# Optimization experiments

Hardware: AMD Instinct MI355X
Metric: run time of the kernel (lower is better)

The kernel has to match this reference:

```python
import jax, jax.numpy as jnp
import numpy as np

N = 100_000      # nodes
E = 1_600_000    # edges (avg degree 16)
D = 128          # emb_dim
L = 2            # num_layer
BN_EPS = 1e-5


def setup_inputs() -> dict:
    key = jax.random.key(0)
    ks = jax.random.split(key, 16)
    s = 0.05
    inp = {
        # int inputs
        "x": jax.random.randint(ks[0], (N, 9), 0, 2),
        "z": jax.random.randint(ks[1], (N,), 0, 1000),
        "edge_index": jax.random.randint(ks[2], (2, E), 0, N),
        "edge_attr": jax.random.randint(ks[3], (E, 3), 0, 2),
        # learned params
        "atom_emb": jax.random.normal(ks[4], (9, 119, D), jnp.float32) * s,  # padded stacked AtomEncoder tables
        "z_emb": jax.random.normal(ks[5], (1000, D), jnp.float32) * s,
        "bond_emb": jax.random.normal(ks[6], (L, 3, 6, D), jnp.float32) * s,  # padded BondEncoder tables per layer
        "eps": jnp.zeros((L,), jnp.float32),
        "W1": jax.random.normal(ks[7], (L, D, 2 * D), jnp.float32) * s,
        "b1": jnp.zeros((L, 2 * D), jnp.float32),
        "g1": jnp.ones((L, 2 * D), jnp.float32),
        "be1": jnp.zeros((L, 2 * D), jnp.float32),
        "W2": jax.random.normal(ks[8], (L, 2 * D, D), jnp.float32) * s,
        "b2": jnp.zeros((L, D), jnp.float32),
        "bng": jnp.ones((L, D), jnp.float32),
        "bnb": jnp.zeros((L, D), jnp.float32),
    }
    return inp


def _batchnorm(h, g, b):
    # training-mode BatchNorm1d: batch stats, biased variance
    m = h.mean(axis=0)
    v = h.var(axis=0)
    return (h - m) * jax.lax.rsqrt(v + BN_EPS) * g + b


def _multi_embed(tables, idx):
    # tables: [F, V, D], idx: [N, F] -> sum_f tables[f][idx[:, f]]  -> [N, D]
    return jax.vmap(lambda t, i: t[i], in_axes=(0, 1))(tables, idx).sum(axis=0)


def reference(x, z, edge_index, edge_attr, atom_emb, z_emb, bond_emb, eps,
              W1, b1, g1, be1, W2, b2, bng, bnb):
    src, dst = edge_index[0], edge_index[1]
    # h0 = AtomEncoder(x) + z_embedding(z)
    h = _multi_embed(atom_emb, x) + z_emb[z]
    for l in range(L):
        # GINConv: bond encode -> gather -> relu message -> scatter-add -> MLP
        e_emb = _multi_embed(bond_emb[l], edge_attr)          # [E, D]
        msg = jax.nn.relu(h[src] + e_emb)                      # [E, D]
        agg = jax.ops.segment_sum(msg, dst, num_segments=N)    # [N, D]
        pre = (1.0 + eps[l]) * h + agg
        hid = jax.nn.relu(_batchnorm(pre @ W1[l] + b1[l], g1[l], be1[l]))
        hconv = hid @ W2[l] + b2[l]
        h = _batchnorm(hconv, bng[l], bnb[l])
        if l < L - 1:
            h = jax.nn.relu(h)   # dropout ratio 0 -> identity
    return h
```

## Files before the change

### kernel.cpp

```cpp
#include <hip/hip_runtime.h>

#define D 128
#define BN_EPS 1e-5f
#define NSUB 1024
#define CAP2 2048
#define NCOPY 64

typedef __attribute__((ext_vector_type(8))) short short8;
typedef __attribute__((ext_vector_type(4))) float floatx4;

__device__ __forceinline__ float bf2f(unsigned short u) {
    unsigned int x = ((unsigned int)u) << 16;
    return __builtin_bit_cast(float, x);
}
__device__ __forceinline__ unsigned short f2bf(float f) {
    unsigned int x = __builtin_bit_cast(unsigned int, f);
    x = x + 0x7FFFu + ((x >> 16) & 1u);
    return (unsigned short)(x >> 16);
}
__device__ __forceinline__ int magdiv(unsigned int x, unsigned long long magic) {
    return (int)(((unsigned long long)x * magic) >> 44);
}

__global__ __launch_bounds__(256)
void partition_kernel(const int* __restrict__ ei, const int* __restrict__ ea,
                      unsigned int* __restrict__ subL, int* __restrict__ tail2,
                      int E, int N, unsigned long long magic, int ntiles, int nblocks) {
    __shared__ int lcnt[1024], lbase[1024];
    const int tid = threadIdx.x;
    for (int tile = blockIdx.x; tile < ntiles; tile += nblocks) {
        const int tb = tile * 4096;
#pragma unroll
        for (int i = 0; i < 4; ++i) lcnt[tid + i * 256] = 0;
        __syncthreads();
        int sub[16];
        unsigned int entry[16];
#pragma unroll
        for (int j = 0; j < 16; ++j) {
            int e = tb + j * 256 + tid;
            if (e < E) {
                int dst = ei[E + e];
                int c = (ea[3 * e] * 6 + ea[3 * e + 1]) * 6 + ea[3 * e + 2];
                int k = magdiv((unsigned)dst * 1024u, magic);
                int lo = (int)(((long long)k * N + 1023) >> 10);
                sub[j] = k;
                entry[j] = (unsigned int)ei[e] | ((unsigned int)c << 17) |
                           ((unsigned int)(dst - lo) << 25);
                atomicAdd(&lcnt[k], 1);
            } else {
                sub[j] = -1;
            }
        }
        __syncthreads();
#pragma unroll
        for (int i = 0; i < 4; ++i) {
            int k = tid + i * 256;
            int c = lcnt[k];
            if (c) lbase[k] = atomicAdd(&tail2[k], c);
            lcnt[k] = 0;
        }
        __syncthreads();
#pragma unroll
        for (int j = 0; j < 16; ++j) {
            if (sub[j] >= 0) {
                int k = sub[j];
                int pos = lbase[k] + atomicAdd(&lcnt[k], 1);
                if (pos < CAP2) subL[(size_t)k * CAP2 + pos] = entry[j];
            }
        }
        __syncthreads();
    }
}

__global__ __launch_bounds__(1024)
void subscan_kernel(const int* __restrict__ tail2, int* __restrict__ subbase,
                    int* __restrict__ offsets, int N) {
    const int tid = threadIdx.x, lane = tid & 63, wid = tid >> 6;
    int v = min(tail2[tid], CAP2);
    int s = v;
#pragma unroll
    for (int off = 1; off < 64; off <<= 1) {
        int t = __shfl_up(s, off, 64);
        if (lane >= off) s += t;
    }
    __shared__ int ws[16];
    if (lane == 63) ws[wid] = s;
    __syncthreads();
    if (wid == 0) {
        int w = (lane < 16) ? ws[lane] : 0;
#pragma unroll
        for (int off = 1; off < 16; off <<= 1) {
            int t = __shfl_up(w, off, 64);
            if (lane >= off) w += t;
        }
        if (lane < 16) ws[lane] = w;
    }
    __syncthreads();
    int excl = (wid ? ws[wid - 1] : 0) + s - v;
    subbase[tid] = excl;
    if (tid == 1023) offsets[N] = excl + v;
}

__global__ __launch_bounds__(256)
void sort_setup_kernel(const unsigned int* __restrict__ subL, const int* __restrict__ tail2,
                       const int* __restrict__ subbase, int* __restrict__ offsets,
                       int* __restrict__ bucket, int N,
                       const int* __restrict__ x, const int* __restrict__ z,
                       const float* __restrict__ atom_emb, const float* __restrict__ z_emb,
                       unsigned short* __restrict__ hb, int nbNode,
                       const float* __restrict__ bond_emb, float* __restrict__ comb,
                       const float* __restrict__ W1, unsigned short* __restrict__ w1p,
                       const float* __restrict__ W2, unsigned short* __restrict__ w2p) {
    __shared__ int cnt[128], loff[128], wsum[4];
    __shared__ unsigned int sorted[CAP2];
    const int tid = threadIdx.x;
    if (blockIdx.x < NSUB) {
        const int k = blockIdx.x;
        const int lane = tid & 63, wid = tid >> 6;
        const int len = min(tail2[k], CAP2);
        const int base = subbase[k];
        const int lo = (int)(((long long)k * N + 1023) >> 10);
        const int hi = (int)(((long long)(k + 1) * N + 1023) >> 10);
        const int nn = hi - lo;
        const unsigned int* src = subL + (size_t)k * CAP2;

        if (tid < 128) cnt[tid] = 0;
        __syncthreads();
        for (int i = tid; i < len; i += 256) atomicAdd(&cnt[src[i] >> 25], 1);
        __syncthreads();
        int v = (tid < 128) ? cnt[tid] : 0;
        int s = v;
#pragma unroll
        for (int off = 1; off < 64; off <<= 1) {
            int t = __shfl_up(s, off, 64);
            if (lane >= off) s += t;
        }
        if (lane == 63) wsum[wid] = s;
        __syncthreads();
        if (tid < 128) loff[tid] = ((wid == 1) ? wsum[0] : 0) + s - v;
        __syncthreads();
        if (tid < nn) offsets[lo + tid] = base + loff[tid];
        if (tid < 128) cnt[tid] = 0;
        __syncthreads();
        for (int i = tid; i < len; i += 256) {
            unsigned int e = src[i];
            int ld = e >> 25;
            int pos = loff[ld] + atomicAdd(&cnt[ld], 1);
            sorted[pos] = e & 0x1FFFFFFu;
        }
        __syncthreads();
        for (int i = tid; i < len; i += 256) bucket[base + i] = (int)sorted[i];
        return;
    }
    const int b = blockIdx.x - NSUB;
    if (b < nbNode) {
        int gid = b * 256 + tid;
        int node = gid >> 5;
        if (node >= N) return;
        int d0 = (gid & 31) * 4;
        float4 acc = *(const float4*)(z_emb + (size_t)z[node] * D + d0);
#pragma unroll
        for (int f = 0; f < 9; ++f) {
            int v = x[node * 9 + f];
            const float4 t = *(const float4*)(atom_emb + (size_t)(f * 119 + v) * D + d0);
            acc.x += t.x; acc.y += t.y; acc.z += t.z; acc.w += t.w;
        }
        ushort4 o;
        o.x = f2bf(acc.x); o.y = f2bf(acc.y); o.z = f2bf(acc.z); o.w = f2bf(acc.w);
        *(ushort4*)(hb + (size_t)node * D + d0) = o;
    } else if (b < nbNode + 216) {
        int t = (b - nbNode) * 256 + tid;
        int layer = t / (216 * D);
        int idx = t - layer * (216 * D);
        int c = idx >> 7, d = idx & 127;
        int a0 = c / 36, a1 = (c / 6) % 6, a2 = c % 6;
        const float* bb = bond_emb + (size_t)layer * 3 * 6 * D;
        float v = bb[(0 * 6 + a0) * D + d] + bb[(1 * 6 + a1) * D + d] + bb[(2 * 6 + a2) * D + d];
        comb[(size_t)layer * 216 * D + idx] = v;
    } else {
        int isW2 = (b >= nbNode + 216 + 256);
        int t = (b - nbNode - 216 - (isW2 ? 256 : 0)) * 256 + tid;
        int layer = t >> 15;
        int idx = t & 32767;
        int logN = isW2 ? 7 : 8;
        int NCOLS = 1 << logN;
        int k = idx >> logN, n = idx & (NCOLS - 1);
        int k0 = k >> 5, kq = k & 31, q = kq >> 3, j = kq & 7;
        int tt = n >> 4, ln = n & 15;
        size_t dest = (((size_t)k0 * (NCOLS >> 4) + tt) << 9) + ((q << 4) + ln) * 8 + j;
        const float* W = (isW2 ? W2 : W1) + (size_t)layer * 32768;
        unsigned short* Wp = (isW2 ? w2p : w1p) + (size_t)layer * 32768;
        Wp[dest] = f2bf(W[idx]);
    }
}

__global__ __launch_bounds__(256)
void gather_reduce_kernel(const int* __restrict__ offsets, const int* __restrict__ bucket,
                          const float* __restrict__ comb,
                          const unsigned short* __restrict__ hb,
                          const float* __restrict__ eps_l,
                          unsigned short* __restrict__ pre, int N) {
    int gid = blockIdx.x * blockDim.x + threadIdx.x;
    int node = gid >> 4;
    if (node >= N) return;
    int d0 = (gid & 15) * 8;

    union U8 { int4 i; unsigned short u[8]; };
    union C8 { float4 v[2]; float f[8]; };
    float s = 1.0f + eps_l[0];
    float a[8];
    {
        U8 hv; hv.i = *(const int4*)(hb + (size_t)node * D + d0);
#pragma unroll
        for (int j = 0; j < 8; ++j) a[j] = bf2f(hv.u[j]) * s;
    }
    const int beg = offsets[node], end = offsets[node + 1];
    for (int p = beg; p < end; p += 4) {
        int rem = end - p;
        int pk0 = bucket[p];
        int pk1 = bucket[rem > 1 ? p + 1 : p];
        int pk2 = bucket[rem > 2 ? p + 2 : p];
        int pk3 = bucket[rem > 3 ? p + 3 : p];
        U8 h0, h1, h2, h3;
        C8 c0, c1, c2, c3;
        h0.i = *(const int4*)(hb + (size_t)(pk0 & 0x1FFFF) * D + d0);
        c0.v[0] = *(const float4*)(comb + (size_t)(pk0 >> 17) * D + d0);
        c0.v[1] = *(const float4*)(comb + (size_t)(pk0 >> 17) * D + d0 + 4);
        h1.i = *(const int4*)(hb + (size_t)(pk1 & 0x1FFFF) * D + d0);
        c1.v[0] = *(const float4*)(comb + (size_t)(pk1 >> 17) * D + d0);
        c1.v[1] = *(const float4*)(comb + (size_t)(pk1 >> 17) * D + d0 + 4);
        h2.i = *(const int4*)(hb + (size_t)(pk2 & 0x1FFFF) * D + d0);
        c2.v[0] = *(const float4*)(comb + (size_t)(pk2 >> 17) * D + d0);
        c2.v[1] = *(const float4*)(comb + (size_t)(pk2 >> 17) * D + d0 + 4);
        h3.i = *(const int4*)(hb + (size_t)(pk3 & 0x1FFFF) * D + d0);
        c3.v[0] = *(const float4*)(comb + (size_t)(pk3 >> 17) * D + d0);
        c3.v[1] = *(const float4*)(comb + (size_t)(pk3 >> 17) * D + d0 + 4);
#pragma unroll
        for (int j = 0; j < 8; ++j) a[j] += fmaxf(bf2f(h0.u[j]) + c0.f[j], 0.0f);
        if (rem > 1) {
#pragma unroll
            for (int j = 0; j < 8; ++j) a[j] += fmaxf(bf2f(h1.u[j]) + c1.f[j], 0.0f);
        }
        if (rem > 2) {
#pragma unroll
            for (int j = 0; j < 8; ++j) a[j] += fmaxf(bf2f(h2.u[j]) + c2.f[j], 0.0f);
        }
        if (rem > 3) {
#pragma unroll
            for (int j = 0; j < 8; ++j) a[j] += fmaxf(bf2f(h3.u[j]) + c3.f[j], 0.0f);
        }
    }
    U8 o;
#pragma unroll
    for (int j = 0; j < 8; ++j) o.u[j] = f2bf(a[j]);
    *(int4*)(pre + (size_t)node * D + d0) = o.i;
}

template <int K, int NCOLS, int TRANSFORM>
__global__ __launch_bounds__(256)
void mfma_gemm_kernel(const unsigned short* __restrict__ A,
                      const unsigned short* __restrict__ Wp,
                      const float* __restrict__ bias,
                      const float* __restrict__ gaccP,
                      const float* __restrict__ gam, const float* __restrict__ bet,
                      float invN,
                      unsigned short* __restrict__ Cbf,
                      float* __restrict__ gacc, int M) {
    constexpr int NT = NCOLS / 16;
    constexpr int NCHUNK = K / 32;
    constexpr int CPP = NCHUNK / 2;
    constexpr int CTS = NCOLS + 8;
    constexpr int WS_SH = (64 * CTS > 16384) ? 64 * CTS : 16384;
    __shared__ unsigned short Ws[WS_SH];
    __shared__ float red[NCOLS * 2];
    __shared__ float tsc_s[TRANSFORM ? K : 1], tsh_s[TRANSFORM ? K : 1];

    const int tid = threadIdx.x;
    const int wave = tid >> 6, lane = tid & 63;
    const int quad = lane >> 4, ln = lane & 15;
    const int m_base = blockIdx.x * 64 + wave * 16;
    int arow = m_base + ln;
    if (arow >= M) arow = M - 1;
    const int kq = quad * 8;

    int4 araw[NCHUNK];
#pragma unroll
    for (int c = 0; c < NCHUNK; ++c)
        araw[c] = *(const int4*)(A + (size_t)arow * K + c * 32 + kq);

    for (int i = tid; i < NCOLS * 2; i += 256) red[i] = 0.f;

    if constexpr (TRANSFORM) {
        for (int col = tid; col < K; col += 256) {
            float s = 0.f, q = 0.f;
            for (int c = 0; c < NCOPY; ++c) {
                const float* p = gaccP + (size_t)c * (K * 2);
                s += p[col];
                q += p[K + col];
            }
            float mean = s * invN;
            float var = q * invN - mean * mean;
            float inv = 1.0f / sqrtf(var + BN_EPS);
            float sc = gam[col] * inv;
            tsc_s[col] = sc;
            tsh_s[col] = bet[col] - mean * sc;
        }
    }

    floatx4 acc[NT];
#pragma unroll
    for (int t = 0; t < NT; ++t) acc[t] = (floatx4){0.f, 0.f, 0.f, 0.f};

#pragma unroll
    for (int ph = 0; ph < 2; ++ph) {
        if (ph) __syncthreads();
#pragma unroll
        for (int i = 0; i < 16384; i += 2048)
            *(int4*)&Ws[i + tid * 8] = *(const int4*)&Wp[ph * 16384 + i + tid * 8];
        __syncthreads();
#pragma unroll
        for (int cc = 0; cc < CPP; ++cc) {
            const int c = ph * CPP + cc;
            short8 afrag;
            if constexpr (TRANSFORM) {
                union { int4 i; unsigned short u[8]; } raw;
                raw.i = araw[c];
                const int kb = c * 32 + kq;
                float4 sc0 = *(const float4*)&tsc_s[kb];
                float4 sc1 = *(const float4*)&tsc_s[kb + 4];
                float4 sh0 = *(const float4*)&tsh_s[kb];
                float4 sh1 = *(const float4*)&tsh_s[kb + 4];
                union { short8 v; unsigned short u[8]; } au;
                au.u[0] = f2bf(fmaxf(bf2f(raw.u[0]) * sc0.x + sh0.x, 0.f));
                au.u[1] = f2bf(fmaxf(bf2f(raw.u[1]) * sc0.y + sh0.y, 0.f));
                au.u[2] = f2bf(fmaxf(bf2f(raw.u[2]) * sc0.z + sh0.z, 0.f));
                au.u[3] = f2bf(fmaxf(bf2f(raw.u[3]) * sc0.w + sh0.w, 0.f));
                au.u[4] = f2bf(fmaxf(bf2f(raw.u[4]) * sc1.x + sh1.x, 0.f));
                au.u[5] = f2bf(fmaxf(bf2f(raw.u[5]) * sc1.y + sh1.y, 0.f));
                au.u[6] = f2bf(fmaxf(bf2f(raw.u[6]) * sc1.z + sh1.z, 0.f));
                au.u[7] = f2bf(fmaxf(bf2f(raw.u[7]) * sc1.w + sh1.w, 0.f));
                afrag = au.v;
            } else {
                afrag = __builtin_bit_cast(short8, araw[c]);
            }
#pragma unroll
            for (int t = 0; t < NT; ++t) {
                short8 bfrag = *(const short8*)&Ws[(((cc * NT) + t) << 9) + lane * 8];
                acc[t] = __builtin_amdgcn_mfma_f32_16x16x32_bf16(afrag, bfrag, acc[t], 0, 0, 0);
            }
        }
    }

    __syncthreads();
#pragma unroll
    for (int t = 0; t < NT; ++t) {
        int col = t * 16 + ln;
        float bv = bias[col];
        float sv = 0.f, qv = 0.f;
#pragma unroll
        for (int r = 0; r < 4; ++r) {
            int lrow = wave * 16 + quad * 4 + r;
            float v = acc[t][r] + bv;
            Ws[lrow * CTS + col] = f2bf(v);
            if (m_base + quad * 4 + r < M) { sv += v; qv += v * v; }
        }
        sv += __shfl_xor(sv, 16, 64); sv += __shfl_xor(sv, 32, 64);
        qv += __shfl_xor(qv, 16, 64); qv += __shfl_xor(qv, 32, 64);
        if (quad == 0) {
            atomicAdd(&red[col], sv);
            atomicAdd(&red[NCOLS + col], qv);
        }
    }
    __syncthreads();
    {
        constexpr int RI4 = NCOLS / 8;
        const int row0 = blockIdx.x * 64;
        unsigned short* cb = Cbf + (size_t)row0 * NCOLS;
        for (int i = tid; i < 64 * RI4; i += 256) {
            int row = i / RI4, cc = i - row * RI4;
            if (row0 + row < M)
                *(int4*)(cb + (size_t)i * 8) = *(const int4*)&Ws[row * CTS + cc * 8];
        }
    }
    float* gout = gacc + (size_t)(blockIdx.x & (NCOPY - 1)) * (NCOLS * 2);
    for (int i = tid; i < NCOLS * 2; i += 256) atomicAdd(&gout[i], red[i]);
}

__global__ __launch_bounds__(256)
void bn_apply_kernel(const unsigned short* __restrict__ Xb,
                     float* __restrict__ Yf, unsigned short* __restrict__ Yb,
                     const float* __restrict__ gacc,
                     const float* __restrict__ g, const float* __restrict__ b,
                     float invN, int N, int mode, int nblocks) {
    __shared__ float sc_s[D], sh_s[D];
    const int tid = threadIdx.x;
    if (tid < D) {
        float s = 0.f, q = 0.f;
        for (int c = 0; c < NCOPY; ++c) {
            const float* p = gacc + (size_t)c * (D * 2);
            s += p[tid];
            q += p[D + tid];
        }
        float mean = s * invN;
        float var = q * invN - mean * mean;
        float inv = 1.0f / sqrtf(var + BN_EPS);
        float sc = g[tid] * inv;
        sc_s[tid] = sc;
        sh_s[tid] = b[tid] - mean * sc;
    }
    __syncthreads();
    const int nchunk = (N + 7) / 8;
    const int d0 = (tid & 31) * 4;
    for (int chunk = blockIdx.x; chunk < nchunk; chunk += nblocks) {
        int node = chunk * 8 + (tid >> 5);
        if (node >= N) continue;
        ushort4 xb = *(const ushort4*)(Xb + (size_t)node * D + d0);
        float4 v;
        v.x = bf2f(xb.x); v.y = bf2f(xb.y); v.z = bf2f(xb.z); v.w = bf2f(xb.w);
        float4 sc = *(const float4*)&sc_s[d0];
        float4 sh = *(const float4*)&sh_s[d0];
        float4 o;
        o.x = v.x * sc.x + sh.x;
        o.y = v.y * sc.y + sh.y;
        o.z = v.z * sc.z + sh.z;
        o.w = v.w * sc.w + sh.w;
        if (mode == 0) {
            ushort4 ob;
            ob.x = f2bf(fmaxf(o.x, 0.f));
            ob.y = f2bf(fmaxf(o.y, 0.f));
            ob.z = f2bf(fmaxf(o.z, 0.f));
            ob.w = f2bf(fmaxf(o.w, 0.f));
            *(ushort4*)(Yb + (size_t)node * D + d0) = ob;
        } else {
            *(float4*)(Yf + (size_t)node * D + d0) = o;
        }
    }
}

extern "C" void kernel_launch(void* const* d_in, const int* in_sizes, int n_in,
                              void* d_out, int out_size, void* d_ws, size_t ws_size,
                              hipStream_t stream) {
    const int*   x        = (const int*)d_in[0];
    const int*   z        = (const int*)d_in[1];
    const int*   ei       = (const int*)d_in[2];
    const int*   ea       = (const int*)d_in[3];
    const float* atom_emb = (const float*)d_in[4];
    const float* z_emb    = (const float*)d_in[5];
    const float* bond_emb = (const float*)d_in[6];
    const float* eps      = (const float*)d_in[7];
    const float* W1       = (const float*)d_in[8];
    const float* b1       = (const float*)d_in[9];
    const float* g1       = (const float*)d_in[10];
    const float* be1      = (const float*)d_in[11];
    const float* W2       = (const float*)d_in[12];
    const float* b2       = (const float*)d_in[13];
    const float* bng      = (const float*)d_in[14];
    const float* bnb      = (const float*)d_in[15];

    const int N = in_sizes[1];
    const int E = in_sizes[3] / 3;

    float* h = (float*)d_out;

    const int ngb = (N + 63) / 64;
    const unsigned long long magic = ((1ULL << 44) / (unsigned int)N) + 1;

    char* ws = (char*)d_ws;
    size_t off = 0;
    auto alloc = [&](size_t bytes) { void* p = ws + off; off += (bytes + 255) & ~(size_t)255; return p; };
    unsigned short* pre_bf = (unsigned short*)alloc((size_t)N * D * 2);
    unsigned short* out2_bf = pre_bf;
    unsigned short* out1_bf = (unsigned short*)alloc((size_t)N * 2 * D * 2);
    unsigned short* hb      = (unsigned short*)alloc((size_t)N * D * 2);
    int* offsets = (int*)alloc((size_t)(N + 1) * 4);
    int* bucket  = (int*)alloc((size_t)E * 4);
    unsigned int* subL = (unsigned int*)alloc((size_t)NSUB * CAP2 * 4);
    int* subbase = (int*)alloc(NSUB * 4);
    float* gstats = (float*)alloc(((size_t)NCOPY * 1536 + 1024) * 4);
    unsigned short* w1p  = (unsigned short*)alloc((size_t)2 * D * 2 * D * 2);
    unsigned short* w2p  = (unsigned short*)alloc((size_t)2 * 2 * D * D * 2);
    float* comb = (float*)alloc((size_t)2 * 216 * D * 4);

    float* gacc1base = gstats;
    float* gacc2base = gstats + (size_t)2 * NCOPY * 512;
    int* tail2 = (int*)(gstats + (size_t)NCOPY * 1536);

    const float invN = 1.0f / (float)N;
    const int ntiles = (E + 4095) / 4096;
    const int nbNode = (N * 32 + 255) / 256;
    const int nbBN = (N + 63) / 64;

    hipMemsetAsync(gstats, 0, ((size_t)NCOPY * 1536 + 1024) * sizeof(float), stream);
    partition_kernel<<<256, 256, 0, stream>>>(ei, ea, subL, tail2, E, N, magic, ntiles, 256);
    subscan_kernel<<<1, 1024, 0, stream>>>(tail2, subbase, offsets, N);
    sort_setup_kernel<<<NSUB + nbNode + 216 + 512, 256, 0, stream>>>(
        subL, tail2, subbase, offsets, bucket, N,
        x, z, atom_emb, z_emb, hb, nbNode, bond_emb, comb, W1, w1p, W2, w2p);

    for (int l = 0; l < 2; ++l) {
        float* gacc1 = gacc1base + (size_t)l * NCOPY * 512;
        float* gacc2 = gacc2base + (size_t)l * NCOPY * 256;

        gather_reduce_kernel<<<(N * 16 + 255) / 256, 256, 0, stream>>>(
            offsets, bucket, comb + (size_t)l * 216 * D, hb, eps + l, pre_bf, N);

        mfma_gemm_kernel<128, 256, 0><<<ngb, 256, 0, stream>>>(
            pre_bf, w1p + (size_t)l * D * 2 * D, b1 + (size_t)l * 2 * D,
            nullptr, nullptr, nullptr, invN, out1_bf, gacc1, N);

        mfma_gemm_kernel<256, 128, 1><<<ngb, 256, 0, stream>>>(
            out1_bf, w2p + (size_t)l * 2 * D * D, b2 + (size_t)l * D,
            gacc1, g1 + (size_t)l * 2 * D, be1 + (size_t)l * 2 * D, invN,
            out2_bf, gacc2, N);

        bn_apply_kernel<<<nbBN, 256, 0, stream>>>(
            out2_bf, h, hb, gacc2, bng + (size_t)l * D, bnb + (size_t)l * D,
            invN, N, l == 0 ? 0 : 1, nbBN);
    }
}
```

Baseline: 483.7 us.

## Fuse layer-0 BatchNorm+ReLU into layer-1 gather and flatten partition grid

After layer 0, the full-size BatchNorm apply pass is replaced by a tiny kernel that computes per-column scale and shift. The layer-1 gather then applies scale, shift and ReLU on the fly to each bf16 row it loads from the GEMM output. This removes one full read and write of the N×D activation array, at the cost of extra FMAs per gathered element, since each node row is read about 16 times. Separately, the partition kernel drops its grid-stride loop and launches one block per 2048-edge tile.

```diff
diff --git a/kernel.cpp b/kernel.cpp
--- a/kernel.cpp
+++ b/kernel.cpp
@@ -25,50 +25,47 @@
 __global__ __launch_bounds__(256)
 void partition_kernel(const int* __restrict__ ei, const int* __restrict__ ea,
                       unsigned int* __restrict__ subL, int* __restrict__ tail2,
-                      int E, int N, unsigned long long magic, int ntiles, int nblocks) {
+                      int E, int N, unsigned long long magic) {
     __shared__ int lcnt[1024], lbase[1024];
     const int tid = threadIdx.x;
-    for (int tile = blockIdx.x; tile < ntiles; tile += nblocks) {
-        const int tb = tile * 4096;
-#pragma unroll
-        for (int i = 0; i < 4; ++i) lcnt[tid + i * 256] = 0;
-        __syncthreads();
-        int sub[16];
-        unsigned int entry[16];
-#pragma unroll
-        for (int j = 0; j < 16; ++j) {
-            int e = tb + j * 256 + tid;
-            if (e < E) {
-                int dst = ei[E + e];
-                int c = (ea[3 * e] * 6 + ea[3 * e + 1]) * 6 + ea[3 * e + 2];
-                int k = magdiv((unsigned)dst * 1024u, magic);
-                int lo = (int)(((long long)k * N + 1023) >> 10);
-                sub[j] = k;
-                entry[j] = (unsigned int)ei[e] | ((unsigned int)c << 17) |
-                           ((unsigned int)(dst - lo) << 25);
-                atomicAdd(&lcnt[k], 1);
-            } else {
-                sub[j] = -1;
-            }
-        }
-        __syncthreads();
-#pragma unroll
-        for (int i = 0; i < 4; ++i) {
-            int k = tid + i * 256;
-            int c = lcnt[k];
-            if (c) lbase[k] = atomicAdd(&tail2[k], c);
-            lcnt[k] = 0;
-        }
-        __syncthreads();
-#pragma unroll
-        for (int j = 0; j < 16; ++j) {
-            if (sub[j] >= 0) {
-                int k = sub[j];
-                int pos = lbase[k] + atomicAdd(&lcnt[k], 1);
-                if (pos < CAP2) subL[(size_t)k * CAP2 + pos] = entry[j];
-            }
-        }
-        __syncthreads();
+    const int tb = blockIdx.x * 2048;
+#pragma unroll
+    for (int i = 0; i < 4; ++i) lcnt[tid + i * 256] = 0;
+    __syncthreads();
+    int sub[8];
+    unsigned int entry[8];
+#pragma unroll
+    for (int j = 0; j < 8; ++j) {
+        int e = tb + j * 256 + tid;
+        if (e < E) {
+            int dst = ei[E + e];
+            int c = (ea[3 * e] * 6 + ea[3 * e + 1]) * 6 + ea[3 * e + 2];
+            int k = magdiv((unsigned)dst * 1024u, magic);
+            int lo = (int)(((long long)k * N + 1023) >> 10);
+            sub[j] = k;
+            entry[j] = (unsigned int)ei[e] | ((unsigned int)c << 17) |
+                       ((unsigned int)(dst - lo) << 25);
+            atomicAdd(&lcnt[k], 1);
+        } else {
+            sub[j] = -1;
+        }
+    }
+    __syncthreads();
+#pragma unroll
+    for (int i = 0; i < 4; ++i) {
+        int k = tid + i * 256;
+        int c = lcnt[k];
+        if (c) lbase[k] = atomicAdd(&tail2[k], c);
+        lcnt[k] = 0;
+    }
+    __syncthreads();
+#pragma unroll
+    for (int j = 0; j < 8; ++j) {
+        if (sub[j] >= 0) {
+            int k = sub[j];
+            int pos = lbase[k] + atomicAdd(&lcnt[k], 1);
+            if (pos < CAP2) subL[(size_t)k * CAP2 + pos] = entry[j];
+        }
     }
 }
 
@@ -194,10 +191,12 @@
     }
 }
 
+template <int GT>
 __global__ __launch_bounds__(256)
 void gather_reduce_kernel(const int* __restrict__ offsets, const int* __restrict__ bucket,
                           const float* __restrict__ comb,
                           const unsigned short* __restrict__ hb,
+                          const float* __restrict__ sc2, const float* __restrict__ sh2,
                           const float* __restrict__ eps_l,
                           unsigned short* __restrict__ pre, int N) {
     int gid = blockIdx.x * blockDim.x + threadIdx.x;
@@ -205,6 +204,19 @@
     if (node >= N) return;
     int d0 = (gid & 15) * 8;
 
+    float scv[8], shv[8];
+    if constexpr (GT) {
+        *(float4*)&scv[0] = *(const float4*)(sc2 + d0);
+        *(float4*)&scv[4] = *(const float4*)(sc2 + d0 + 4);
+        *(float4*)&shv[0] = *(const float4*)(sh2 + d0);
+        *(float4*)&shv[4] = *(const float4*)(sh2 + d0 + 4);
+    }
+    auto tf = [&](unsigned short u, int j) -> float {
+        float xv = bf2f(u);
+        if constexpr (GT) xv = fmaxf(xv * scv[j] + shv[j], 0.f);
+        return xv;
+    };
+
     union U8 { int4 i; unsigned short u[8]; };
     union C8 { float4 v[2]; float f[8]; };
     float s = 1.0f + eps_l[0];
@@ -212,7 +224,7 @@
     {
         U8 hv; hv.i = *(const int4*)(hb + (size_t)node * D + d0);
 #pragma unroll
-        for (int j = 0; j < 8; ++j) a[j] = bf2f(hv.u[j]) * s;
+        for (int j = 0; j < 8; ++j) a[j] = tf(hv.u[j], j) * s;
     }
     const int beg = offsets[node], end = offsets[node + 1];
     for (int p = beg; p < end; p += 4) {
@@ -236,18 +248,18 @@
         c3.v[0] = *(const float4*)(comb + (size_t)(pk3 >> 17) * D + d0);
         c3.v[1] = *(const float4*)(comb + (size_t)(pk3 >> 17) * D + d0 + 4);
 #pragma unroll
-        for (int j = 0; j < 8; ++j) a[j] += fmaxf(bf2f(h0.u[j]) + c0.f[j], 0.0f);
+        for (int j = 0; j < 8; ++j) a[j] += fmaxf(tf(h0.u[j], j) + c0.f[j], 0.0f);
         if (rem > 1) {
 #pragma unroll
-            for (int j = 0; j < 8; ++j) a[j] += fmaxf(bf2f(h1.u[j]) + c1.f[j], 0.0f);
+            for (int j = 0; j < 8; ++j) a[j] += fmaxf(tf(h1.u[j], j) + c1.f[j], 0.0f);
         }
         if (rem > 2) {
 #pragma unroll
-            for (int j = 0; j < 8; ++j) a[j] += fmaxf(bf2f(h2.u[j]) + c2.f[j], 0.0f);
+            for (int j = 0; j < 8; ++j) a[j] += fmaxf(tf(h2.u[j], j) + c2.f[j], 0.0f);
         }
         if (rem > 3) {
 #pragma unroll
-            for (int j = 0; j < 8; ++j) a[j] += fmaxf(bf2f(h3.u[j]) + c3.f[j], 0.0f);
+            for (int j = 0; j < 8; ++j) a[j] += fmaxf(tf(h3.u[j], j) + c3.f[j], 0.0f);
         }
     }
     U8 o;
@@ -386,12 +398,34 @@
     for (int i = tid; i < NCOLS * 2; i += 256) atomicAdd(&gout[i], red[i]);
 }
 
+template <int NCOLS>
+__global__ void stats_final_kernel(const float* __restrict__ gacc,
+                                   const float* __restrict__ g, const float* __restrict__ b,
+                                   float* __restrict__ scale, float* __restrict__ shift,
+                                   float invN) {
+    int col = threadIdx.x;
+    if (col < NCOLS) {
+        float s = 0.f, q = 0.f;
+        for (int c = 0; c < NCOPY; ++c) {
+            const float* p = gacc + (size_t)c * (NCOLS * 2);
+            s += p[col];
+            q += p[NCOLS + col];
+        }
+        float mean = s * invN;
+        float var = q * invN - mean * mean;
+        float inv = 1.0f / sqrtf(var + BN_EPS);
+        float sc = g[col] * inv;
+        scale[col] = sc;
+        shift[col] = b[col] - mean * sc;
+    }
+}
+
 __global__ __launch_bounds__(256)
 void bn_apply_kernel(const unsigned short* __restrict__ Xb,
-                     float* __restrict__ Yf, unsigned short* __restrict__ Yb,
+                     float* __restrict__ Yf,
                      const float* __restrict__ gacc,
                      const float* __restrict__ g, const float* __restrict__ b,
-                     float invN, int N, int mode, int nblocks) {
+                     float invN, int N, int nblocks) {
     __shared__ float sc_s[D], sh_s[D];
     const int tid = threadIdx.x;
     if (tid < D) {
@@ -424,16 +458,7 @@
         o.y = v.y * sc.y + sh.y;
         o.z = v.z * sc.z + sh.z;
         o.w = v.w * sc.w + sh.w;
-        if (mode == 0) {
-            ushort4 ob;
-            ob.x = f2bf(fmaxf(o.x, 0.f));
-            ob.y = f2bf(fmaxf(o.y, 0.f));
-            ob.z = f2bf(fmaxf(o.z, 0.f));
-            ob.w = f2bf(fmaxf(o.w, 0.f));
-            *(ushort4*)(Yb + (size_t)node * D + d0) = ob;
-        } else {
-            *(float4*)(Yf + (size_t)node * D + d0) = o;
-        }
+        *(float4*)(Yf + (size_t)node * D + d0) = o;
     }
 }
 
@@ -468,30 +493,33 @@
     char* ws = (char*)d_ws;
     size_t off = 0;
     auto alloc = [&](size_t bytes) { void* p = ws + off; off += (bytes + 255) & ~(size_t)255; return p; };
-    unsigned short* pre_bf = (unsigned short*)alloc((size_t)N * D * 2);
-    unsigned short* out2_bf = pre_bf;
+    unsigned short* pre_bf  = (unsigned short*)alloc((size_t)N * D * 2);
+    unsigned short* out2_bf = (unsigned short*)alloc((size_t)N * D * 2);
     unsigned short* out1_bf = (unsigned short*)alloc((size_t)N * 2 * D * 2);
     unsigned short* hb      = (unsigned short*)alloc((size_t)N * D * 2);
     int* offsets = (int*)alloc((size_t)(N + 1) * 4);
     int* bucket  = (int*)alloc((size_t)E * 4);
     unsigned int* subL = (unsigned int*)alloc((size_t)NSUB * CAP2 * 4);
     int* subbase = (int*)alloc(NSUB * 4);
+    float* stats = (float*)alloc(256 * 4);
     float* gstats = (float*)alloc(((size_t)NCOPY * 1536 + 1024) * 4);
     unsigned short* w1p  = (unsigned short*)alloc((size_t)2 * D * 2 * D * 2);
     unsigned short* w2p  = (unsigned short*)alloc((size_t)2 * 2 * D * D * 2);
     float* comb = (float*)alloc((size_t)2 * 216 * D * 4);
 
+    float* scale2 = stats;
+    float* shift2 = stats + 128;
     float* gacc1base = gstats;
     float* gacc2base = gstats + (size_t)2 * NCOPY * 512;
     int* tail2 = (int*)(gstats + (size_t)NCOPY * 1536);
 
     const float invN = 1.0f / (float)N;
-    const int ntiles = (E + 4095) / 4096;
+    const int ntiles = (E + 2047) / 2048;
     const int nbNode = (N * 32 + 255) / 256;
     const int nbBN = (N + 63) / 64;
 
     hipMemsetAsync(gstats, 0, ((size_t)NCOPY * 1536 + 1024) * sizeof(float), stream);
-    partition_kernel<<<256, 256, 0, stream>>>(ei, ea, subL, tail2, E, N, magic, ntiles, 256);
+    partition_kernel<<<ntiles, 256, 0, stream>>>(ei, ea, subL, tail2, E, N, magic);
     subscan_kernel<<<1, 1024, 0, stream>>>(tail2, subbase, offsets, N);
     sort_setup_kernel<<<NSUB + nbNode + 216 + 512, 256, 0, stream>>>(
         subL, tail2, subbase, offsets, bucket, N,
@@ -501,8 +529,14 @@
         float* gacc1 = gacc1base + (size_t)l * NCOPY * 512;
         float* gacc2 = gacc2base + (size_t)l * NCOPY * 256;
 
-        gather_reduce_kernel<<<(N * 16 + 255) / 256, 256, 0, stream>>>(
-            offsets, bucket, comb + (size_t)l * 216 * D, hb, eps + l, pre_bf, N);
+        if (l == 0) {
+            gather_reduce_kernel<0><<<(N * 16 + 255) / 256, 256, 0, stream>>>(
+                offsets, bucket, comb, hb, nullptr, nullptr, eps, pre_bf, N);
+        } else {
+            gather_reduce_kernel<1><<<(N * 16 + 255) / 256, 256, 0, stream>>>(
+                offsets, bucket, comb + (size_t)216 * D, out2_bf, scale2, shift2,
+                eps + 1, pre_bf, N);
+        }
 
         mfma_gemm_kernel<128, 256, 0><<<ngb, 256, 0, stream>>>(
             pre_bf, w1p + (size_t)l * D * 2 * D, b1 + (size_t)l * 2 * D,
@@ -513,8 +547,13 @@
             gacc1, g1 + (size_t)l * 2 * D, be1 + (size_t)l * 2 * D, invN,
             out2_bf, gacc2, N);
 
-        bn_apply_kernel<<<nbBN, 256, 0, stream>>>(
-            out2_bf, h, hb, gacc2, bng + (size_t)l * D, bnb + (size_t)l * D,
-            invN, N, l == 0 ? 0 : 1, nbBN);
-    }
-}
+        if (l == 0) {
+            stats_final_kernel<128><<<1, 128, 0, stream>>>(
+                gacc2, bng, bnb, scale2, shift2, invN);
+        } else {
+            bn_apply_kernel<<<nbBN, 256, 0, stream>>>(
+                out2_bf, h, gacc2, bng + (size_t)l * D, bnb + (size_t)l * D,
+                invN, N, nbBN);
+        }
+    }
+}
```

New measurement: 482.4 us. No clear change (-0.3%).

## Sort edges per tile in LDS before writing partition buckets, one tile per block

Applied to the files above, without the earlier changes.

The partition kernel now runs one 4096-edge tile per block instead of a grid-stride loop. It scans the local bucket counts and stages the entries sorted by bucket in shared memory, so each bucket's run is written to global memory as a contiguous block rather than as scattered per-thread stores. The bn_apply launch also shrinks to a fixed 256 blocks. The trade-off is an extra block-level scan and serial per-bucket copy loops, whose lengths can be uneven across threads.

```diff
diff --git a/kernel.cpp b/kernel.cpp
--- a/kernel.cpp
+++ b/kernel.cpp
@@ -5,6 +5,7 @@
 #define NSUB 1024
 #define CAP2 2048
 #define NCOPY 64
+#define PTILE 4096
 
 typedef __attribute__((ext_vector_type(8))) short short8;
 typedef __attribute__((ext_vector_type(4))) float floatx4;
@@ -25,50 +26,79 @@
 __global__ __launch_bounds__(256)
 void partition_kernel(const int* __restrict__ ei, const int* __restrict__ ea,
                       unsigned int* __restrict__ subL, int* __restrict__ tail2,
-                      int E, int N, unsigned long long magic, int ntiles, int nblocks) {
-    __shared__ int lcnt[1024], lbase[1024];
+                      int E, int N, unsigned long long magic) {
+    __shared__ int lcnt[1024], loff[1024];
+    __shared__ unsigned int sorted[PTILE];
+    __shared__ int wsum2[4];
     const int tid = threadIdx.x;
-    for (int tile = blockIdx.x; tile < ntiles; tile += nblocks) {
-        const int tb = tile * 4096;
-#pragma unroll
-        for (int i = 0; i < 4; ++i) lcnt[tid + i * 256] = 0;
-        __syncthreads();
-        int sub[16];
-        unsigned int entry[16];
-#pragma unroll
-        for (int j = 0; j < 16; ++j) {
-            int e = tb + j * 256 + tid;
-            if (e < E) {
-                int dst = ei[E + e];
-                int c = (ea[3 * e] * 6 + ea[3 * e + 1]) * 6 + ea[3 * e + 2];
-                int k = magdiv((unsigned)dst * 1024u, magic);
-                int lo = (int)(((long long)k * N + 1023) >> 10);
-                sub[j] = k;
-                entry[j] = (unsigned int)ei[e] | ((unsigned int)c << 17) |
-                           ((unsigned int)(dst - lo) << 25);
-                atomicAdd(&lcnt[k], 1);
-            } else {
-                sub[j] = -1;
+    const int tb = blockIdx.x * PTILE;
+#pragma unroll
+    for (int i = 0; i < 4; ++i) lcnt[tid + i * 256] = 0;
+    __syncthreads();
+    int sub[16];
+    unsigned int entry[16];
+#pragma unroll
+    for (int j = 0; j < 16; ++j) {
+        int e = tb + j * 256 + tid;
+        if (e < E) {
+            int dst = ei[E + e];
+            int c = (ea[3 * e] * 6 + ea[3 * e + 1]) * 6 + ea[3 * e + 2];
+            int k = magdiv((unsigned)dst * 1024u, magic);
+            int lo = (int)(((long long)k * N + 1023) >> 10);
+            sub[j] = k;
+            entry[j] = (unsigned int)ei[e] | ((unsigned int)c << 17) |
+                       ((unsigned int)(dst - lo) << 25);
+            atomicAdd(&lcnt[k], 1);
+        } else {
+            sub[j] = -1;
+        }
+    }
+    __syncthreads();
+    int c4[4], tsum = 0;
+#pragma unroll
+    for (int j = 0; j < 4; ++j) { c4[j] = lcnt[tid * 4 + j]; tsum += c4[j]; }
+    {
+        const int lane = tid & 63, wid = tid >> 6;
+        int s = tsum;
+#pragma unroll
+        for (int off = 1; off < 64; off <<= 1) {
+            int t = __shfl_up(s, off, 64);
+            if (lane >= off) s += t;
+        }
+        if (lane == 63) wsum2[wid] = s;
+        __syncthreads();
+        int woff = 0;
+        for (int w = 0; w < wid; ++w) woff += wsum2[w];
+        int run = woff + s - tsum;
+#pragma unroll
+        for (int j = 0; j < 4; ++j) { loff[tid * 4 + j] = run; run += c4[j]; }
+    }
+    __syncthreads();
+#pragma unroll
+    for (int i = 0; i < 4; ++i) lcnt[tid + i * 256] = 0;
+    __syncthreads();
+#pragma unroll
+    for (int j = 0; j < 16; ++j) {
+        if (sub[j] >= 0) {
+            int k = sub[j];
+            int idx = atomicAdd(&lcnt[k], 1);
+            sorted[loff[k] + idx] = entry[j];
+        }
+    }
+    __syncthreads();
+#pragma unroll
+    for (int j = 0; j < 4; ++j) {
+        int k = tid * 4 + j;
+        int c = lcnt[k];
+        if (c) {
+            int gb = atomicAdd(&tail2[k], c);
+            int lb = loff[k];
+            unsigned int* dstp = subL + (size_t)k * CAP2;
+            for (int i = 0; i < c; ++i) {
+                int pos = gb + i;
+                if (pos < CAP2) dstp[pos] = sorted[lb + i];
             }
         }
-        __syncthreads();
-#pragma unroll
-        for (int i = 0; i < 4; ++i) {
-            int k = tid + i * 256;
-            int c = lcnt[k];
-            if (c) lbase[k] = atomicAdd(&tail2[k], c);
-            lcnt[k] = 0;
-        }
-        __syncthreads();
-#pragma unroll
-        for (int j = 0; j < 16; ++j) {
-            if (sub[j] >= 0) {
-                int k = sub[j];
-                int pos = lbase[k] + atomicAdd(&lcnt[k], 1);
-                if (pos < CAP2) subL[(size_t)k * CAP2 + pos] = entry[j];
-            }
-        }
-        __syncthreads();
     }
 }
 
@@ -486,12 +516,11 @@
     int* tail2 = (int*)(gstats + (size_t)NCOPY * 1536);
 
     const float invN = 1.0f / (float)N;
-    const int ntiles = (E + 4095) / 4096;
+    const int ntiles = (E + PTILE - 1) / PTILE;
     const int nbNode = (N * 32 + 255) / 256;
-    const int nbBN = (N + 63) / 64;
 
     hipMemsetAsync(gstats, 0, ((size_t)NCOPY * 1536 + 1024) * sizeof(float), stream);
-    partition_kernel<<<256, 256, 0, stream>>>(ei, ea, subL, tail2, E, N, magic, ntiles, 256);
+    partition_kernel<<<ntiles, 256, 0, stream>>>(ei, ea, subL, tail2, E, N, magic);
     subscan_kernel<<<1, 1024, 0, stream>>>(tail2, subbase, offsets, N);
     sort_setup_kernel<<<NSUB + nbNode + 216 + 512, 256, 0, stream>>>(
         subL, tail2, subbase, offsets, bucket, N,
@@ -513,8 +542,8 @@
             gacc1, g1 + (size_t)l * 2 * D, be1 + (size_t)l * 2 * D, invN,
             out2_bf, gacc2, N);
 
-        bn_apply_kernel<<<nbBN, 256, 0, stream>>>(
+        bn_apply_kernel<<<256, 256, 0, stream>>>(
             out2_bf, h, hb, gacc2, bng + (size_t)l * D, bnb + (size_t)l * D,
-            invN, N, l == 0 ? 0 : 1, nbBN);
-    }
-}
+            invN, N, l == 0 ? 0 : 1, 256);
+    }
+}
```

New measurement: 505.4 us. 1.04x slower.
